# Optimization experiments

Measured on AMD Instinct MI355X. Metric: run time of the kernel, lower is better.

The kernel has to match this reference:

```python
import jax, jax.numpy as jnp
import numpy as np
from jax import lax

B, D_IN, LOW_DIM, NUM_CLASS, MOCO_QUEUE = 4096, 1024, 128, 32, 65536
PROTO_M, MOCO_M, EPS = 0.99, 0.999, 1e-12


def l2norm(x, axis=-1):
    n = jnp.linalg.norm(x, axis=axis, keepdims=True)
    return x / jnp.maximum(n, EPS)


def encoder(x, W_cls, b_cls, W_proj):
    # base_encoder returns (class logits, l2-normalized low-dim embedding)
    return x @ W_cls + b_cls, l2norm(x @ W_proj)


def setup_inputs() -> dict:
    key = jax.random.key(0)
    k = jax.random.split(key, 12)
    img_q = jax.random.normal(k[0], (B, D_IN), jnp.float32)
    im_k = jax.random.normal(k[1], (B, D_IN), jnp.float32)
    true_lab = jax.random.randint(k[2], (B,), 0, NUM_CLASS)
    partial_Y = (jax.random.uniform(k[3], (B, NUM_CLASS)) < 0.3).astype(jnp.float32)
    partial_Y = partial_Y.at[jnp.arange(B), true_lab].set(1.0)  # guarantee nonempty candidate set
    W_cls_q = 0.02 * jax.random.normal(k[4], (D_IN, NUM_CLASS), jnp.float32)
    b_cls_q = jnp.zeros((NUM_CLASS,), jnp.float32)
    W_proj_q = 0.02 * jax.random.normal(k[5], (D_IN, LOW_DIM), jnp.float32)
    # key encoder initialized near query encoder (copied then momentum-drifted)
    W_cls_k = W_cls_q + 0.002 * jax.random.normal(k[6], (D_IN, NUM_CLASS), jnp.float32)
    b_cls_k = jnp.zeros((NUM_CLASS,), jnp.float32)
    W_proj_k = W_proj_q + 0.002 * jax.random.normal(k[7], (D_IN, LOW_DIM), jnp.float32)
    queue = jax.random.normal(k[8], (MOCO_QUEUE, LOW_DIM), jnp.float32)
    queue = queue / jnp.maximum(jnp.linalg.norm(queue, axis=0, keepdims=True), EPS)  # F.normalize(queue, dim=0) as in __init__
    queue_pseudo = jax.random.normal(k[9], (MOCO_QUEUE, NUM_CLASS), jnp.float32)
    queue_partial = jax.random.normal(k[10], (MOCO_QUEUE, NUM_CLASS), jnp.float32)
    prototypes = l2norm(jax.random.normal(k[11], (NUM_CLASS, LOW_DIM), jnp.float32))
    return dict(img_q=img_q, im_k=im_k, partial_Y=partial_Y,
                W_cls_q=W_cls_q, b_cls_q=b_cls_q, W_proj_q=W_proj_q,
                W_cls_k=W_cls_k, b_cls_k=b_cls_k, W_proj_k=W_proj_k,
                prototypes=prototypes, queue=queue,
                queue_pseudo=queue_pseudo, queue_partial=queue_partial)


def reference(img_q, im_k, partial_Y, W_cls_q, b_cls_q, W_proj_q,
              W_cls_k, b_cls_k, W_proj_k, prototypes, queue,
              queue_pseudo, queue_partial):
    output, q = encoder(img_q, W_cls_q, b_cls_q, W_proj_q)
    predicted_scores = jax.nn.softmax(output, axis=1) * partial_Y
    pseudo_labels = jnp.argmax(predicted_scores, axis=1)  # (B,) int
    # prototypes are detached before the similarity (clone().detach())
    score_prot = jax.nn.softmax(q @ lax.stop_gradient(prototypes).T, axis=1)
    # order-dependent per-sample EMA scatter (faithful to the python for-loop,
    # including within-batch label collisions) -> lax.scan recurrence
    qd = lax.stop_gradient(q)
    def step(p, xs):
        feat, lab = xs
        return p.at[lab].set(p[lab] * PROTO_M + (1.0 - PROTO_M) * feat), None
    new_protos, _ = lax.scan(step, lax.stop_gradient(prototypes), (qd, pseudo_labels))
    new_protos = l2norm(new_protos)
    # momentum key-encoder update (no grad), then key features
    Wck = lax.stop_gradient(W_cls_k * MOCO_M + W_cls_q * (1.0 - MOCO_M))
    bck = lax.stop_gradient(b_cls_k * MOCO_M + b_cls_q * (1.0 - MOCO_M))
    Wpk = lax.stop_gradient(W_proj_k * MOCO_M + W_proj_q * (1.0 - MOCO_M))
    _, kfeat = encoder(im_k, Wck, bck, Wpk)
    kfeat = lax.stop_gradient(kfeat)
    qv = lax.stop_gradient(queue)
    qp = lax.stop_gradient(queue_pseudo)
    qpt = lax.stop_gradient(queue_partial)
    features = jnp.concatenate([q, kfeat, qv], axis=0)
    pseudo_scores = jnp.concatenate([predicted_scores, predicted_scores, qp], axis=0)
    partial_target = jnp.concatenate([partial_Y, partial_Y, qpt], axis=0)
    # dequeue-and-enqueue at ptr=0 (buffer state update, no grad)
    new_queue = qv.at[0:B].set(kfeat)
    new_queue_pseudo = qp.at[0:B].set(lax.stop_gradient(predicted_scores))
    new_queue_partial = qpt.at[0:B].set(lax.stop_gradient(partial_Y))
    return (output, features, pseudo_scores, partial_target, score_prot,
            new_protos, new_queue, new_queue_pseudo, new_queue_partial)
```

## Files before the change

### kernel.cpp

```cpp
#include <hip/hip_runtime.h>
#include <hip/hip_bf16.h>
#include <stdint.h>


typedef __attribute__((ext_vector_type(8))) short bf16x8;
typedef __attribute__((ext_vector_type(4))) float f32x4;

constexpr size_t O0 = 0;
constexpr size_t O1 = 131072;
constexpr size_t O2 = 9568256;
constexpr size_t O3 = 11927552;
constexpr size_t O4 = 14286848;
constexpr size_t O5 = 14417920;
constexpr size_t O6 = 14422016;
constexpr size_t O7 = 22810624;
constexpr size_t O8 = 24907776;

__device__ __forceinline__ unsigned short f2b(float x) {
  union { float f; uint32_t u; } v; v.f = x;
  uint32_t u = v.u;
  uint32_t r = (u + 0x7fffu + ((u >> 16) & 1u)) >> 16;
  return (unsigned short)r;
}

__global__ __launch_bounds__(256) void prep_w(const float* __restrict__ W1,
                                              const float* __restrict__ W2,
                                              float a1, float a2, int N,
                                              unsigned short* __restrict__ Wt) {
  __shared__ float tile[32][33];
  const int kb = blockIdx.x * 32, nb = blockIdx.y * 32;
  const int tx = threadIdx.x, ty = threadIdx.y;
#pragma unroll
  for (int j = 0; j < 4; ++j) {
    const int k = kb + ty + 8 * j;
    float v = W1[(size_t)k * N + nb + tx] * a1;
    if (W2) v += W2[(size_t)k * N + nb + tx] * a2;
    tile[ty + 8 * j][tx] = v;
  }
  __syncthreads();
#pragma unroll
  for (int j = 0; j < 4; ++j) {
    const int n = nb + ty + 8 * j;
    Wt[(size_t)n * 1024 + kb + tx] = f2b(tile[tx][ty + 8 * j]);
  }
}

template <int NWAVES>
__global__ __launch_bounds__(NWAVES * 64) void gemm_enc(
    const float* __restrict__ A, const unsigned short* __restrict__ Wt,
    float* __restrict__ C) {
  constexpr int BN = NWAVES * 32;
  constexpr int NT = NWAVES * 64;
  constexpr int K = 1024;
  __shared__ __align__(16) unsigned char sA[16 * 128];
  __shared__ __align__(16) unsigned char sB[BN * 128];
  const int t = threadIdx.x;
  const int w = t >> 6, l = t & 63;
  const int ar = l & 15, kg = l >> 4;
  const int cs = w * 32;
  const int m0 = blockIdx.x * 16;
  f32x4 acc0 = {0.f, 0.f, 0.f, 0.f}, acc1 = {0.f, 0.f, 0.f, 0.f};
  for (int k0 = 0; k0 < K; k0 += 64) {
    if (t < 256) {
      const int r = t >> 4;
      const int c8 = (t & 15) * 8;
      const float4 v = *(const float4*)(A + (size_t)(m0 + r) * K + k0 + (t & 15) * 4);
      uint2 pk;
      pk.x = (uint32_t)f2b(v.x) | ((uint32_t)f2b(v.y) << 16);
      pk.y = (uint32_t)f2b(v.z) | ((uint32_t)f2b(v.w) << 16);
      *(uint2*)(sA + ((r * 128 + c8) ^ ((r & 7) << 4))) = pk;
    }
#pragma unroll
    for (int i = 0; i < (BN * 8) / NT; ++i) {
      const int cid = t + i * NT;
      const int r = cid >> 3, c = cid & 7;
      const uint4 v = *(const uint4*)(Wt + (size_t)r * K + k0 + c * 8);
      *(uint4*)(sB + ((r * 128 + c * 16) ^ ((r & 7) << 4))) = v;
    }
    __syncthreads();
#pragma unroll
    for (int s = 0; s < 2; ++s) {
      const int ch = (s * 4 + kg) * 16;
      bf16x8 a = *(const bf16x8*)(sA + ((ar * 128 + ch) ^ ((ar & 7) << 4)));
      const int r0 = cs + ar, r1 = cs + 16 + ar;
      bf16x8 b0 = *(const bf16x8*)(sB + ((r0 * 128 + ch) ^ ((r0 & 7) << 4)));
      bf16x8 b1 = *(const bf16x8*)(sB + ((r1 * 128 + ch) ^ ((r1 & 7) << 4)));
      acc0 = __builtin_amdgcn_mfma_f32_16x16x32_bf16(a, b0, acc0, 0, 0, 0);
      acc1 = __builtin_amdgcn_mfma_f32_16x16x32_bf16(a, b1, acc1, 0, 0, 0);
    }
    __syncthreads();
  }
#pragma unroll
  for (int j = 0; j < 4; ++j) {
    const int row = m0 + kg * 4 + j;
    C[(size_t)row * BN + cs + ar] = acc0[j];
    C[(size_t)row * BN + cs + 16 + ar] = acc1[j];
  }
}

__global__ __launch_bounds__(256) void post_q(
    const float* __restrict__ CQ, const float* __restrict__ bias,
    const float* __restrict__ partialY, const float* __restrict__ protos,
    float* __restrict__ out, int* __restrict__ labels) {
  __shared__ float pr[32 * 129];
  __shared__ float qs[4][128];
  const int t = threadIdx.x;
  for (int i = t; i < 4096; i += 256) pr[(i >> 7) * 129 + (i & 127)] = protos[i];
  __syncthreads();
  const int w = t >> 6, l = t & 63;
  const int row = blockIdx.x * 4 + w;
  const float* cq = CQ + (size_t)row * 160;

  float logit = -1e30f;
  if (l < 32) logit = cq[128 + l] + bias[l];
  float m = logit;
  for (int o = 32; o; o >>= 1) m = fmaxf(m, __shfl_xor(m, o));
  const float e = (l < 32) ? __expf(logit - m) : 0.f;
  float ssum = e;
  for (int o = 32; o; o >>= 1) ssum += __shfl_xor(ssum, o);
  const float py = (l < 32) ? partialY[(size_t)row * 32 + l] : 0.f;
  const float p = e / ssum * py;
  if (l < 32) {
    out[O0 + (size_t)row * 32 + l] = logit;
    out[O2 + (size_t)row * 32 + l] = p;
    out[O2 + (size_t)(4096 + row) * 32 + l] = p;
    out[O7 + (size_t)row * 32 + l] = p;
    out[O3 + (size_t)row * 32 + l] = py;
    out[O3 + (size_t)(4096 + row) * 32 + l] = py;
    out[O8 + (size_t)row * 32 + l] = py;
  }
  float av = (l < 32) ? p : -1.f;
  int ai = (l < 32) ? l : 1000;
  for (int o = 32; o; o >>= 1) {
    const float ov = __shfl_xor(av, o);
    const int oi = __shfl_xor(ai, o);
    if (ov > av || (ov == av && oi < ai)) { av = ov; ai = oi; }
  }
  if (l == 0) labels[row] = ai;

  float v0 = cq[l], v1 = cq[64 + l];
  float ss = v0 * v0 + v1 * v1;
  for (int o = 32; o; o >>= 1) ss += __shfl_xor(ss, o);
  const float den = fmaxf(sqrtf(ss), 1e-12f);
  v0 /= den; v1 /= den;
  out[O1 + (size_t)row * 128 + l] = v0;
  out[O1 + (size_t)row * 128 + 64 + l] = v1;
  qs[w][l] = v0;
  qs[w][64 + l] = v1;

  const int c = l & 31;
  const int dh = (l >> 5) * 64;
  float acc = 0.f;
#pragma unroll
  for (int d = 0; d < 64; ++d) acc += qs[w][dh + d] * pr[c * 129 + dh + d];
  acc += __shfl_xor(acc, 32);
  float sm = acc;
  for (int o = 16; o; o >>= 1) sm = fmaxf(sm, __shfl_xor(sm, o));
  const float ee = __expf(acc - sm);
  float s2 = ee;
  for (int o = 16; o; o >>= 1) s2 += __shfl_xor(s2, o);
  if (l < 32) out[O4 + (size_t)row * 32 + l] = ee / s2;
}

__global__ __launch_bounds__(256) void post_k(const float* __restrict__ CK,
                                              float* __restrict__ out) {
  const int t = threadIdx.x, w = t >> 6, l = t & 63;
  const int row = blockIdx.x * 4 + w;
  const float* ck = CK + (size_t)row * 128;
  float v0 = ck[l], v1 = ck[64 + l];
  float ss = v0 * v0 + v1 * v1;
  for (int o = 32; o; o >>= 1) ss += __shfl_xor(ss, o);
  const float den = fmaxf(sqrtf(ss), 1e-12f);
  v0 /= den; v1 /= den;
  out[O1 + (size_t)(4096 + row) * 128 + l] = v0;
  out[O1 + (size_t)(4096 + row) * 128 + 64 + l] = v1;
  out[O6 + (size_t)row * 128 + l] = v0;
  out[O6 + (size_t)row * 128 + 64 + l] = v1;
}

__global__ __launch_bounds__(128) void proto_up(const int* __restrict__ labels,
                                                const float* __restrict__ qfeat,
                                                const float* __restrict__ protos,
                                                float* __restrict__ out) {
  __shared__ int lab[4096];
  __shared__ int list[4096];
  __shared__ int cnt[128];
  __shared__ int ktot;
  __shared__ float red[2];
  const int c = blockIdx.x, t = threadIdx.x;
  for (int i = t; i < 4096; i += 128) lab[i] = labels[i];
  __syncthreads();
  int cn = 0;
#pragma unroll
  for (int j = 0; j < 32; ++j) {
    const int jj = (j + t) & 31;
    cn += (lab[t * 32 + jj] == c) ? 1 : 0;
  }
  cnt[t] = cn;
  __syncthreads();
  if (t == 0) {
    int s = 0;
    for (int i = 0; i < 128; ++i) { const int v = cnt[i]; cnt[i] = s; s += v; }
    ktot = s;
  }
  __syncthreads();
  int off = cnt[t];
  for (int j = 0; j < 32; ++j) {
    const int i = t * 32 + j;
    if (lab[i] == c) list[off++] = i;
  }
  __syncthreads();
  const int k = ktot;
  float* wf = (float*)lab;
  for (int j = t; j < k; j += 128)
    wf[j] = 0.01f * __powf(0.99f, (float)(k - 1 - j));
  __syncthreads();
  float acc = protos[(size_t)c * 128 + t] * __powf(0.99f, (float)k);
  for (int j = 0; j < k; ++j)
    acc += wf[j] * qfeat[(size_t)list[j] * 128 + t];
  float ss = acc * acc;
  for (int o = 32; o; o >>= 1) ss += __shfl_xor(ss, o);
  if ((t & 63) == 0) red[t >> 6] = ss;
  __syncthreads();
  const float tot = red[0] + red[1];
  out[O5 + (size_t)c * 128 + t] = acc / fmaxf(sqrtf(tot), 1e-12f);
}

__global__ __launch_bounds__(256) void copy_bufs(const float* __restrict__ queue,
                                                 const float* __restrict__ qp,
                                                 const float* __restrict__ qpt,
                                                 float* __restrict__ out) {
  constexpr long NQ4 = (long)65536 * 128 / 4;
  constexpr long NP4 = (long)65536 * 32 / 4;
  constexpr long TOT = NQ4 + 2 * NP4;
  float4* o4 = (float4*)out;
  for (long idx = (long)blockIdx.x * blockDim.x + threadIdx.x; idx < TOT;
       idx += (long)gridDim.x * blockDim.x) {
    if (idx < NQ4) {
      const float4 v = ((const float4*)queue)[idx];
      o4[O1 / 4 + (2L * 4096 * 128) / 4 + idx] = v;
      if ((idx >> 5) >= 4096) o4[O6 / 4 + idx] = v;
    } else if (idx < NQ4 + NP4) {
      const long i = idx - NQ4;
      const float4 v = ((const float4*)qp)[i];
      o4[O2 / 4 + (2L * 4096 * 32) / 4 + i] = v;
      if ((i >> 3) >= 4096) o4[O7 / 4 + i] = v;
    } else {
      const long i = idx - NQ4 - NP4;
      const float4 v = ((const float4*)qpt)[i];
      o4[O3 / 4 + (2L * 4096 * 32) / 4 + i] = v;
      if ((i >> 3) >= 4096) o4[O8 / 4 + i] = v;
    }
  }
}

extern "C" void kernel_launch(void* const* d_in, const int* in_sizes, int n_in,
                              void* d_out, int out_size, void* d_ws, size_t ws_size,
                              hipStream_t stream) {
  const float* img_q    = (const float*)d_in[0];
  const float* im_k     = (const float*)d_in[1];
  const float* partialY = (const float*)d_in[2];
  const float* W_cls_q  = (const float*)d_in[3];
  const float* b_cls_q  = (const float*)d_in[4];
  const float* W_proj_q = (const float*)d_in[5];
  const float* W_proj_k = (const float*)d_in[8];
  const float* protos   = (const float*)d_in[9];
  const float* queue    = (const float*)d_in[10];
  const float* queue_ps = (const float*)d_in[11];
  const float* queue_pt = (const float*)d_in[12];
  float* out = (float*)d_out;

  unsigned short* wtq = (unsigned short*)d_ws;
  unsigned short* wtk = wtq + 160 * 1024;
  float* CQ = (float*)(wtk + 128 * 1024);
  float* CK = CQ + (size_t)4096 * 160;
  int* labels = (int*)(CK + (size_t)4096 * 128);

  prep_w<<<dim3(32, 4), dim3(32, 8), 0, stream>>>(W_proj_q, nullptr, 1.0f, 0.0f, 128, wtq);
  prep_w<<<dim3(32, 1), dim3(32, 8), 0, stream>>>(W_cls_q, nullptr, 1.0f, 0.0f, 32, wtq + 128 * 1024);
  prep_w<<<dim3(32, 4), dim3(32, 8), 0, stream>>>(W_proj_k, W_proj_q, 0.999f, 0.001f, 128, wtk);
  gemm_enc<5><<<256, 320, 0, stream>>>(img_q, wtq, CQ);
  gemm_enc<4><<<256, 256, 0, stream>>>(im_k, wtk, CK);
  post_q<<<1024, 256, 0, stream>>>(CQ, b_cls_q, partialY, protos, out, labels);
  post_k<<<1024, 256, 0, stream>>>(CK, out);
  proto_up<<<32, 128, 0, stream>>>(labels, out + O1, protos, out);
  copy_bufs<<<2048, 256, 0, stream>>>(queue, queue_ps, queue_pt, out);
}
```

Baseline: 262.6 us.

## Fuse encoder GEMMs with epilogues and merge prep and tail kernels

Replaces nine launches with three: one weight-prep kernel, one GEMM kernel that handles both query and key encoders and runs the softmax/normalize/prototype-score epilogue in-block from shared memory, and one tail kernel combining the prototype update with the queue copies. It also register-double-buffers the global loads in the GEMM main loop and uses a wave-scan for the per-class label compaction. The intent is to cut launch overhead and avoid round-tripping the GEMM outputs through global memory. The cost is a larger shared-memory footprint, idle waves in key blocks, and more complex code.

```diff
diff --git a/kernel.cpp b/kernel.cpp
--- a/kernel.cpp
+++ b/kernel.cpp
@@ -23,233 +23,306 @@
   return (unsigned short)r;
 }
 
-__global__ __launch_bounds__(256) void prep_w(const float* __restrict__ W1,
-                                              const float* __restrict__ W2,
-                                              float a1, float a2, int N,
-                                              unsigned short* __restrict__ Wt) {
+#define SWZ(r, cb) ((((r) * 128) + (cb)) ^ (((r) & 7) << 4))
+
+__global__ __launch_bounds__(256) void prep(
+    const float* __restrict__ Wpq, const float* __restrict__ Wcq,
+    const float* __restrict__ Wpk,
+    unsigned short* __restrict__ wt_q, unsigned short* __restrict__ wt_pk) {
+  const int bid = blockIdx.x;
+  const int t = threadIdx.x;
+  const float *W1, *W2 = nullptr;
+  float a1 = 1.f, a2 = 0.f;
+  unsigned short* dst;
+  int kb, nbr, nbw, N;
+  if (bid < 128) {
+    W1 = Wpq; N = 128; kb = (bid & 31) * 32; nbr = nbw = (bid >> 5) * 32;
+    dst = wt_q;
+  } else if (bid < 160) {
+    W1 = Wcq; N = 32; kb = (bid - 128) * 32; nbr = 0; nbw = 128; dst = wt_q;
+  } else {
+    W1 = Wpk; W2 = Wpq; a1 = 0.999f; a2 = 0.001f; N = 128;
+    const int b = bid - 160; kb = (b & 31) * 32; nbr = nbw = (b >> 5) * 32;
+    dst = wt_pk;
+  }
   __shared__ float tile[32][33];
-  const int kb = blockIdx.x * 32, nb = blockIdx.y * 32;
-  const int tx = threadIdx.x, ty = threadIdx.y;
+  const int tx = t & 31, ty = t >> 5;
 #pragma unroll
   for (int j = 0; j < 4; ++j) {
     const int k = kb + ty + 8 * j;
-    float v = W1[(size_t)k * N + nb + tx] * a1;
-    if (W2) v += W2[(size_t)k * N + nb + tx] * a2;
+    float v = W1[(size_t)k * N + nbr + tx] * a1;
+    if (W2) v += W2[(size_t)k * N + nbr + tx] * a2;
     tile[ty + 8 * j][tx] = v;
   }
   __syncthreads();
 #pragma unroll
   for (int j = 0; j < 4; ++j) {
-    const int n = nb + ty + 8 * j;
-    Wt[(size_t)n * 1024 + kb + tx] = f2b(tile[tx][ty + 8 * j]);
-  }
-}
-
-template <int NWAVES>
-__global__ __launch_bounds__(NWAVES * 64) void gemm_enc(
-    const float* __restrict__ A, const unsigned short* __restrict__ Wt,
-    float* __restrict__ C) {
-  constexpr int BN = NWAVES * 32;
-  constexpr int NT = NWAVES * 64;
-  constexpr int K = 1024;
-  __shared__ __align__(16) unsigned char sA[16 * 128];
-  __shared__ __align__(16) unsigned char sB[BN * 128];
+    const int n = nbw + ty + 8 * j;
+    dst[(size_t)n * 1024 + kb + tx] = f2b(tile[tx][ty + 8 * j]);
+  }
+}
+
+__global__ __launch_bounds__(320) void gemm_fused(
+    const float* __restrict__ img_q, const float* __restrict__ im_k,
+    const unsigned short* __restrict__ wt_q,
+    const unsigned short* __restrict__ wt_pk,
+    const float* __restrict__ bias, const float* __restrict__ partialY,
+    const float* __restrict__ protos, float* __restrict__ out,
+    int* __restrict__ labels) {
+  __shared__ __align__(16) unsigned char smem[28672];
+  unsigned char* sA = smem;
+  unsigned char* sB = smem + 2048;
+  const int bid = blockIdx.x;
   const int t = threadIdx.x;
   const int w = t >> 6, l = t & 63;
   const int ar = l & 15, kg = l >> 4;
-  const int cs = w * 32;
-  const int m0 = blockIdx.x * 16;
+  const bool isq = bid < 256;
+  const int m0 = (isq ? bid : bid - 256) * 16;
+  const float* A = isq ? img_q : im_k;
+  const unsigned short* Wt = isq ? wt_q : wt_pk;
+  const int BROWS8 = isq ? 1280 : 1024;
+  const int arow = t >> 4, acol = t & 15;
+
+  float4 avA, avB;
+  uint4 bvA[4], bvB[4];
+  if (t < 256) {
+    avA = *(const float4*)(A + (size_t)(m0 + arow) * 1024 + acol * 4);
+    avB = *(const float4*)(A + (size_t)(m0 + arow) * 1024 + 64 + acol * 4);
+  }
+#pragma unroll
+  for (int i = 0; i < 4; ++i) {
+    const int cid = t + i * 320;
+    if (cid < BROWS8) {
+      const int r = cid >> 3, c = cid & 7;
+      bvA[i] = *(const uint4*)(Wt + (size_t)r * 1024 + c * 8);
+      bvB[i] = *(const uint4*)(Wt + (size_t)r * 1024 + 64 + c * 8);
+    }
+  }
   f32x4 acc0 = {0.f, 0.f, 0.f, 0.f}, acc1 = {0.f, 0.f, 0.f, 0.f};
-  for (int k0 = 0; k0 < K; k0 += 64) {
-    if (t < 256) {
-      const int r = t >> 4;
-      const int c8 = (t & 15) * 8;
-      const float4 v = *(const float4*)(A + (size_t)(m0 + r) * K + k0 + (t & 15) * 4);
-      uint2 pk;
-      pk.x = (uint32_t)f2b(v.x) | ((uint32_t)f2b(v.y) << 16);
-      pk.y = (uint32_t)f2b(v.z) | ((uint32_t)f2b(v.w) << 16);
-      *(uint2*)(sA + ((r * 128 + c8) ^ ((r & 7) << 4))) = pk;
-    }
-#pragma unroll
-    for (int i = 0; i < (BN * 8) / NT; ++i) {
-      const int cid = t + i * NT;
-      const int r = cid >> 3, c = cid & 7;
-      const uint4 v = *(const uint4*)(Wt + (size_t)r * K + k0 + c * 8);
-      *(uint4*)(sB + ((r * 128 + c * 16) ^ ((r & 7) << 4))) = v;
-    }
-    __syncthreads();
-#pragma unroll
-    for (int s = 0; s < 2; ++s) {
-      const int ch = (s * 4 + kg) * 16;
-      bf16x8 a = *(const bf16x8*)(sA + ((ar * 128 + ch) ^ ((ar & 7) << 4)));
-      const int r0 = cs + ar, r1 = cs + 16 + ar;
-      bf16x8 b0 = *(const bf16x8*)(sB + ((r0 * 128 + ch) ^ ((r0 & 7) << 4)));
-      bf16x8 b1 = *(const bf16x8*)(sB + ((r1 * 128 + ch) ^ ((r1 & 7) << 4)));
-      acc0 = __builtin_amdgcn_mfma_f32_16x16x32_bf16(a, b0, acc0, 0, 0, 0);
-      acc1 = __builtin_amdgcn_mfma_f32_16x16x32_bf16(a, b1, acc1, 0, 0, 0);
-    }
-    __syncthreads();
-  }
-#pragma unroll
-  for (int j = 0; j < 4; ++j) {
-    const int row = m0 + kg * 4 + j;
-    C[(size_t)row * BN + cs + ar] = acc0[j];
-    C[(size_t)row * BN + cs + 16 + ar] = acc1[j];
-  }
-}
-
-__global__ __launch_bounds__(256) void post_q(
-    const float* __restrict__ CQ, const float* __restrict__ bias,
-    const float* __restrict__ partialY, const float* __restrict__ protos,
-    float* __restrict__ out, int* __restrict__ labels) {
-  __shared__ float pr[32 * 129];
-  __shared__ float qs[4][128];
+
+#define STAGE(av, bv)                                                        \
+  {                                                                          \
+    if (t < 256) {                                                           \
+      uint2 pk;                                                              \
+      pk.x = (uint32_t)f2b(av.x) | ((uint32_t)f2b(av.y) << 16);              \
+      pk.y = (uint32_t)f2b(av.z) | ((uint32_t)f2b(av.w) << 16);              \
+      *(uint2*)(sA + SWZ(arow, acol * 8)) = pk;                              \
+    }                                                                        \
+    _Pragma("unroll") for (int i = 0; i < 4; ++i) {                          \
+      const int cid = t + i * 320;                                           \
+      if (cid < BROWS8) {                                                    \
+        const int r = cid >> 3, c = cid & 7;                                 \
+        *(uint4*)(sB + SWZ(r, c * 16)) = bv[i];                              \
+      }                                                                      \
+    }                                                                        \
+  }
+#define RELOAD(av, bv, kt)                                                   \
+  {                                                                          \
+    const int k0 = (kt) * 64;                                                \
+    if (t < 256)                                                             \
+      av = *(const float4*)(A + (size_t)(m0 + arow) * 1024 + k0 + acol * 4); \
+    _Pragma("unroll") for (int i = 0; i < 4; ++i) {                          \
+      const int cid = t + i * 320;                                           \
+      if (cid < BROWS8) {                                                    \
+        const int r = cid >> 3, c = cid & 7;                                 \
+        bv[i] = *(const uint4*)(Wt + (size_t)r * 1024 + k0 + c * 8);         \
+      }                                                                      \
+    }                                                                        \
+  }
+#define MFMA_PHASE()                                                         \
+  if (isq || w < 4) {                                                        \
+    _Pragma("unroll") for (int s = 0; s < 2; ++s) {                          \
+      const int ch = (s * 4 + kg) * 16;                                      \
+      bf16x8 a = *(const bf16x8*)(sA + SWZ(ar, ch));                         \
+      const int r0 = w * 32 + ar, r1 = w * 32 + 16 + ar;                     \
+      bf16x8 b0 = *(const bf16x8*)(sB + SWZ(r0, ch));                        \
+      bf16x8 b1 = *(const bf16x8*)(sB + SWZ(r1, ch));                        \
+      acc0 = __builtin_amdgcn_mfma_f32_16x16x32_bf16(a, b0, acc0, 0, 0, 0);  \
+      acc1 = __builtin_amdgcn_mfma_f32_16x16x32_bf16(a, b1, acc1, 0, 0, 0);  \
+    }                                                                        \
+  }
+
+  for (int it = 0; it < 16; it += 2) {
+    STAGE(avA, bvA);
+    if (it + 2 < 16) RELOAD(avA, bvA, it + 2);
+    __syncthreads();
+    MFMA_PHASE();
+    __syncthreads();
+    STAGE(avB, bvB);
+    if (it + 3 < 16) RELOAD(avB, bvB, it + 3);
+    __syncthreads();
+    MFMA_PHASE();
+    __syncthreads();
+  }
+
+  float* pr = (float*)smem;
+  float* Crow = (float*)(smem + 16512);
+  if (isq || w < 4) {
+#pragma unroll
+    for (int j = 0; j < 4; ++j) {
+      Crow[(kg * 4 + j) * 164 + w * 32 + ar] = acc0[j];
+      Crow[(kg * 4 + j) * 164 + w * 32 + 16 + ar] = acc1[j];
+    }
+  }
+  if (isq) {
+    for (int i = t; i < 4096; i += 320)
+      pr[(i >> 7) * 129 + (i & 127)] = protos[i];
+  }
+  __syncthreads();
+
+  if (isq) {
+    for (int r = w; r < 16; r += 5) {
+      const int grow = m0 + r;
+      const float* cr = Crow + r * 164;
+      float logit = -1e30f;
+      if (l < 32) logit = cr[128 + l] + bias[l];
+      float m = logit;
+      for (int o = 32; o; o >>= 1) m = fmaxf(m, __shfl_xor(m, o));
+      const float e = (l < 32) ? __expf(logit - m) : 0.f;
+      float ssum = e;
+      for (int o = 32; o; o >>= 1) ssum += __shfl_xor(ssum, o);
+      const float py = (l < 32) ? partialY[(size_t)grow * 32 + l] : 0.f;
+      const float p = e / ssum * py;
+      if (l < 32) {
+        out[O0 + (size_t)grow * 32 + l] = logit;
+        out[O2 + (size_t)grow * 32 + l] = p;
+        out[O2 + (size_t)(4096 + grow) * 32 + l] = p;
+        out[O7 + (size_t)grow * 32 + l] = p;
+        out[O3 + (size_t)grow * 32 + l] = py;
+        out[O3 + (size_t)(4096 + grow) * 32 + l] = py;
+        out[O8 + (size_t)grow * 32 + l] = py;
+      }
+      float av = (l < 32) ? p : -1.f;
+      int ai = (l < 32) ? l : 1000;
+      for (int o = 32; o; o >>= 1) {
+        const float ov = __shfl_xor(av, o);
+        const int oi = __shfl_xor(ai, o);
+        if (ov > av || (ov == av && oi < ai)) { av = ov; ai = oi; }
+      }
+      if (l == 0) labels[grow] = ai;
+      float v0 = cr[l], v1 = cr[64 + l];
+      float ss = v0 * v0 + v1 * v1;
+      for (int o = 32; o; o >>= 1) ss += __shfl_xor(ss, o);
+      const float den = fmaxf(sqrtf(ss), 1e-12f);
+      v0 /= den; v1 /= den;
+      out[O1 + (size_t)grow * 128 + l] = v0;
+      out[O1 + (size_t)grow * 128 + 64 + l] = v1;
+      Crow[r * 164 + l] = v0;
+      Crow[r * 164 + 64 + l] = v1;
+      const int c = l & 31;
+      const int dh = (l >> 5) * 64;
+      float acc = 0.f;
+#pragma unroll
+      for (int d = 0; d < 64; ++d)
+        acc += Crow[r * 164 + dh + d] * pr[c * 129 + dh + d];
+      acc += __shfl_xor(acc, 32);
+      float sm = acc;
+      for (int o = 16; o; o >>= 1) sm = fmaxf(sm, __shfl_xor(sm, o));
+      const float ee = __expf(acc - sm);
+      float s2 = ee;
+      for (int o = 16; o; o >>= 1) s2 += __shfl_xor(s2, o);
+      if (l < 32) out[O4 + (size_t)grow * 32 + l] = ee / s2;
+    }
+  } else if (w < 4) {
+    for (int r = w; r < 16; r += 4) {
+      const int grow = m0 + r;
+      const float* cr = Crow + r * 164;
+      float v0 = cr[l], v1 = cr[64 + l];
+      float ss = v0 * v0 + v1 * v1;
+      for (int o = 32; o; o >>= 1) ss += __shfl_xor(ss, o);
+      const float den = fmaxf(sqrtf(ss), 1e-12f);
+      v0 /= den; v1 /= den;
+      out[O1 + (size_t)(4096 + grow) * 128 + l] = v0;
+      out[O1 + (size_t)(4096 + grow) * 128 + 64 + l] = v1;
+      out[O6 + (size_t)grow * 128 + l] = v0;
+      out[O6 + (size_t)grow * 128 + 64 + l] = v1;
+    }
+  }
+}
+
+__global__ __launch_bounds__(256) void tail_all(
+    const float* __restrict__ queue, const float* __restrict__ qp,
+    const float* __restrict__ qpt, const int* __restrict__ labels,
+    const float* __restrict__ protos, float* __restrict__ out) {
+  const int bid = blockIdx.x;
   const int t = threadIdx.x;
-  for (int i = t; i < 4096; i += 256) pr[(i >> 7) * 129 + (i & 127)] = protos[i];
-  __syncthreads();
-  const int w = t >> 6, l = t & 63;
-  const int row = blockIdx.x * 4 + w;
-  const float* cq = CQ + (size_t)row * 160;
-
-  float logit = -1e30f;
-  if (l < 32) logit = cq[128 + l] + bias[l];
-  float m = logit;
-  for (int o = 32; o; o >>= 1) m = fmaxf(m, __shfl_xor(m, o));
-  const float e = (l < 32) ? __expf(logit - m) : 0.f;
-  float ssum = e;
-  for (int o = 32; o; o >>= 1) ssum += __shfl_xor(ssum, o);
-  const float py = (l < 32) ? partialY[(size_t)row * 32 + l] : 0.f;
-  const float p = e / ssum * py;
-  if (l < 32) {
-    out[O0 + (size_t)row * 32 + l] = logit;
-    out[O2 + (size_t)row * 32 + l] = p;
-    out[O2 + (size_t)(4096 + row) * 32 + l] = p;
-    out[O7 + (size_t)row * 32 + l] = p;
-    out[O3 + (size_t)row * 32 + l] = py;
-    out[O3 + (size_t)(4096 + row) * 32 + l] = py;
-    out[O8 + (size_t)row * 32 + l] = py;
-  }
-  float av = (l < 32) ? p : -1.f;
-  int ai = (l < 32) ? l : 1000;
-  for (int o = 32; o; o >>= 1) {
-    const float ov = __shfl_xor(av, o);
-    const int oi = __shfl_xor(ai, o);
-    if (ov > av || (ov == av && oi < ai)) { av = ov; ai = oi; }
-  }
-  if (l == 0) labels[row] = ai;
-
-  float v0 = cq[l], v1 = cq[64 + l];
-  float ss = v0 * v0 + v1 * v1;
-  for (int o = 32; o; o >>= 1) ss += __shfl_xor(ss, o);
-  const float den = fmaxf(sqrtf(ss), 1e-12f);
-  v0 /= den; v1 /= den;
-  out[O1 + (size_t)row * 128 + l] = v0;
-  out[O1 + (size_t)row * 128 + 64 + l] = v1;
-  qs[w][l] = v0;
-  qs[w][64 + l] = v1;
-
-  const int c = l & 31;
-  const int dh = (l >> 5) * 64;
-  float acc = 0.f;
-#pragma unroll
-  for (int d = 0; d < 64; ++d) acc += qs[w][dh + d] * pr[c * 129 + dh + d];
-  acc += __shfl_xor(acc, 32);
-  float sm = acc;
-  for (int o = 16; o; o >>= 1) sm = fmaxf(sm, __shfl_xor(sm, o));
-  const float ee = __expf(acc - sm);
-  float s2 = ee;
-  for (int o = 16; o; o >>= 1) s2 += __shfl_xor(s2, o);
-  if (l < 32) out[O4 + (size_t)row * 32 + l] = ee / s2;
-}
-
-__global__ __launch_bounds__(256) void post_k(const float* __restrict__ CK,
-                                              float* __restrict__ out) {
-  const int t = threadIdx.x, w = t >> 6, l = t & 63;
-  const int row = blockIdx.x * 4 + w;
-  const float* ck = CK + (size_t)row * 128;
-  float v0 = ck[l], v1 = ck[64 + l];
-  float ss = v0 * v0 + v1 * v1;
-  for (int o = 32; o; o >>= 1) ss += __shfl_xor(ss, o);
-  const float den = fmaxf(sqrtf(ss), 1e-12f);
-  v0 /= den; v1 /= den;
-  out[O1 + (size_t)(4096 + row) * 128 + l] = v0;
-  out[O1 + (size_t)(4096 + row) * 128 + 64 + l] = v1;
-  out[O6 + (size_t)row * 128 + l] = v0;
-  out[O6 + (size_t)row * 128 + 64 + l] = v1;
-}
-
-__global__ __launch_bounds__(128) void proto_up(const int* __restrict__ labels,
-                                                const float* __restrict__ qfeat,
-                                                const float* __restrict__ protos,
-                                                float* __restrict__ out) {
-  __shared__ int lab[4096];
-  __shared__ int list[4096];
-  __shared__ int cnt[128];
-  __shared__ int ktot;
-  __shared__ float red[2];
-  const int c = blockIdx.x, t = threadIdx.x;
-  for (int i = t; i < 4096; i += 128) lab[i] = labels[i];
-  __syncthreads();
-  int cn = 0;
-#pragma unroll
-  for (int j = 0; j < 32; ++j) {
-    const int jj = (j + t) & 31;
-    cn += (lab[t * 32 + jj] == c) ? 1 : 0;
-  }
-  cnt[t] = cn;
-  __syncthreads();
-  if (t == 0) {
-    int s = 0;
-    for (int i = 0; i < 128; ++i) { const int v = cnt[i]; cnt[i] = s; s += v; }
-    ktot = s;
-  }
-  __syncthreads();
-  int off = cnt[t];
-  for (int j = 0; j < 32; ++j) {
-    const int i = t * 32 + j;
-    if (lab[i] == c) list[off++] = i;
-  }
-  __syncthreads();
-  const int k = ktot;
-  float* wf = (float*)lab;
-  for (int j = t; j < k; j += 128)
-    wf[j] = 0.01f * __powf(0.99f, (float)(k - 1 - j));
-  __syncthreads();
-  float acc = protos[(size_t)c * 128 + t] * __powf(0.99f, (float)k);
-  for (int j = 0; j < k; ++j)
-    acc += wf[j] * qfeat[(size_t)list[j] * 128 + t];
-  float ss = acc * acc;
-  for (int o = 32; o; o >>= 1) ss += __shfl_xor(ss, o);
-  if ((t & 63) == 0) red[t >> 6] = ss;
-  __syncthreads();
-  const float tot = red[0] + red[1];
-  out[O5 + (size_t)c * 128 + t] = acc / fmaxf(sqrtf(tot), 1e-12f);
-}
-
-__global__ __launch_bounds__(256) void copy_bufs(const float* __restrict__ queue,
-                                                 const float* __restrict__ qp,
-                                                 const float* __restrict__ qpt,
-                                                 float* __restrict__ out) {
-  constexpr long NQ4 = (long)65536 * 128 / 4;
-  constexpr long NP4 = (long)65536 * 32 / 4;
-  constexpr long TOT = NQ4 + 2 * NP4;
-  float4* o4 = (float4*)out;
-  for (long idx = (long)blockIdx.x * blockDim.x + threadIdx.x; idx < TOT;
-       idx += (long)gridDim.x * blockDim.x) {
-    if (idx < NQ4) {
-      const float4 v = ((const float4*)queue)[idx];
-      o4[O1 / 4 + (2L * 4096 * 128) / 4 + idx] = v;
-      if ((idx >> 5) >= 4096) o4[O6 / 4 + idx] = v;
-    } else if (idx < NQ4 + NP4) {
-      const long i = idx - NQ4;
-      const float4 v = ((const float4*)qp)[i];
-      o4[O2 / 4 + (2L * 4096 * 32) / 4 + i] = v;
-      if ((i >> 3) >= 4096) o4[O7 / 4 + i] = v;
-    } else {
-      const long i = idx - NQ4 - NP4;
-      const float4 v = ((const float4*)qpt)[i];
-      o4[O3 / 4 + (2L * 4096 * 32) / 4 + i] = v;
-      if ((i >> 3) >= 4096) o4[O8 / 4 + i] = v;
+  if (bid < 32) {
+    __shared__ int lab[4096];
+    __shared__ int list[4096];
+    __shared__ int wtot[4];
+    __shared__ float red[2];
+    const int c = bid;
+    const int w = t >> 6, l = t & 63;
+    for (int i = t; i < 4096; i += 256) lab[i] = labels[i];
+    __syncthreads();
+    int cn = 0;
+#pragma unroll
+    for (int j = 0; j < 16; ++j) {
+      const int jj = (j + t) & 15;
+      cn += (lab[t * 16 + jj] == c) ? 1 : 0;
+    }
+    int inc = cn;
+    for (int o = 1; o < 64; o <<= 1) {
+      const int n = __shfl_up(inc, o);
+      if (l >= o) inc += n;
+    }
+    if (l == 63) wtot[w] = inc;
+    __syncthreads();
+    int base = 0;
+    for (int ww = 0; ww < w; ++ww) base += wtot[ww];
+    const int k = wtot[0] + wtot[1] + wtot[2] + wtot[3];
+    int off = base + inc - cn;
+    for (int j = 0; j < 16; ++j) {
+      const int i = t * 16 + j;
+      if (lab[i] == c) list[off++] = i;
+    }
+    __syncthreads();
+    float* wf = (float*)lab;
+    for (int j = t; j < k; j += 256)
+      wf[j] = 0.01f * __powf(0.99f, (float)(k - 1 - j));
+    __syncthreads();
+    float acc = 0.f;
+    if (t < 128) {
+      const float* qfeat = out + O1;
+      float a0 = protos[(size_t)c * 128 + t] * __powf(0.99f, (float)k);
+      float a1 = 0.f, a2 = 0.f, a3 = 0.f;
+      int j = 0;
+      for (; j + 4 <= k; j += 4) {
+        a0 += wf[j]     * qfeat[(size_t)list[j] * 128 + t];
+        a1 += wf[j + 1] * qfeat[(size_t)list[j + 1] * 128 + t];
+        a2 += wf[j + 2] * qfeat[(size_t)list[j + 2] * 128 + t];
+        a3 += wf[j + 3] * qfeat[(size_t)list[j + 3] * 128 + t];
+      }
+      for (; j < k; ++j) a0 += wf[j] * qfeat[(size_t)list[j] * 128 + t];
+      acc = (a0 + a1) + (a2 + a3);
+      float ss = acc * acc;
+      for (int o = 32; o; o >>= 1) ss += __shfl_xor(ss, o);
+      if ((t & 63) == 0) red[t >> 6] = ss;
+    }
+    __syncthreads();
+    if (t < 128)
+      out[O5 + (size_t)c * 128 + t] = acc / fmaxf(sqrtf(red[0] + red[1]), 1e-12f);
+  } else {
+    constexpr long NQ4 = (long)65536 * 128 / 4;
+    constexpr long NP4 = (long)65536 * 32 / 4;
+    constexpr long TOT = NQ4 + 2 * NP4;
+    float4* o4 = (float4*)out;
+    for (long idx = (long)(bid - 32) * 256 + t; idx < TOT; idx += 3072L * 256) {
+      if (idx < NQ4) {
+        const float4 v = ((const float4*)queue)[idx];
+        o4[O1 / 4 + (2L * 4096 * 128) / 4 + idx] = v;
+        if ((idx >> 5) >= 4096) o4[O6 / 4 + idx] = v;
+      } else if (idx < NQ4 + NP4) {
+        const long i = idx - NQ4;
+        const float4 v = ((const float4*)qp)[i];
+        o4[O2 / 4 + (2L * 4096 * 32) / 4 + i] = v;
+        if ((i >> 3) >= 4096) o4[O7 / 4 + i] = v;
+      } else {
+        const long i = idx - NQ4 - NP4;
+        const float4 v = ((const float4*)qpt)[i];
+        o4[O3 / 4 + (2L * 4096 * 32) / 4 + i] = v;
+        if ((i >> 3) >= 4096) o4[O8 / 4 + i] = v;
+      }
     }
   }
 }
@@ -270,19 +343,13 @@
   const float* queue_pt = (const float*)d_in[12];
   float* out = (float*)d_out;
 
-  unsigned short* wtq = (unsigned short*)d_ws;
-  unsigned short* wtk = wtq + 160 * 1024;
-  float* CQ = (float*)(wtk + 128 * 1024);
-  float* CK = CQ + (size_t)4096 * 160;
-  int* labels = (int*)(CK + (size_t)4096 * 128);
-
-  prep_w<<<dim3(32, 4), dim3(32, 8), 0, stream>>>(W_proj_q, nullptr, 1.0f, 0.0f, 128, wtq);
-  prep_w<<<dim3(32, 1), dim3(32, 8), 0, stream>>>(W_cls_q, nullptr, 1.0f, 0.0f, 32, wtq + 128 * 1024);
-  prep_w<<<dim3(32, 4), dim3(32, 8), 0, stream>>>(W_proj_k, W_proj_q, 0.999f, 0.001f, 128, wtk);
-  gemm_enc<5><<<256, 320, 0, stream>>>(img_q, wtq, CQ);
-  gemm_enc<4><<<256, 256, 0, stream>>>(im_k, wtk, CK);
-  post_q<<<1024, 256, 0, stream>>>(CQ, b_cls_q, partialY, protos, out, labels);
-  post_k<<<1024, 256, 0, stream>>>(CK, out);
-  proto_up<<<32, 128, 0, stream>>>(labels, out + O1, protos, out);
-  copy_bufs<<<2048, 256, 0, stream>>>(queue, queue_ps, queue_pt, out);
-}
+  unsigned short* wt_q  = (unsigned short*)d_ws;
+  unsigned short* wt_pk = wt_q + 160 * 1024;
+  int* labels = (int*)(wt_pk + 128 * 1024);
+
+  prep<<<288, 256, 0, stream>>>(W_proj_q, W_cls_q, W_proj_k, wt_q, wt_pk);
+  gemm_fused<<<512, 320, 0, stream>>>(img_q, im_k, wt_q, wt_pk, b_cls_q,
+                                      partialY, protos, out, labels);
+  tail_all<<<3104, 256, 0, stream>>>(queue, queue_ps, queue_pt, labels,
+                                     protos, out);
+}
```

Result: slower. 279.9 us (+6.6%).
